# Kernel optimization log

Hardware: AMD Instinct MI355X
Metric: run time of the kernel (lower is better)

The kernel has to match this reference:

```python
import jax, jax.numpy as jnp
import numpy as np

N = 8192
D_IN = 512
D_HID = 256
D_OUT = 128
NEG_SLOPE = 0.25
MASK_VAL = -1.0e12
EDGE_PROB = 0.004  # avg degree ~33


def _leaky(x):
    return jax.nn.leaky_relu(x, NEG_SLOPE)


def setup_inputs() -> dict:
    key = jax.random.key(0)
    ks = jax.random.split(key, 9)
    x = jax.random.normal(ks[0], (N, D_IN), jnp.float32)
    # sparse-ish normalized adjacency, stored dense (torch uses sparse mm / to_dense)
    vals = jax.random.uniform(ks[1], (N, N), jnp.float32)
    mask = jax.random.uniform(ks[2], (N, N)) < EDGE_PROB
    adj = jnp.where(mask, vals, 0.0).astype(jnp.float32)
    W1 = jax.random.normal(ks[3], (D_IN, D_HID), jnp.float32) * (2.0 / (D_IN + D_HID)) ** 0.5
    b1 = jnp.zeros((D_HID,), jnp.float32)
    W2 = jax.random.normal(ks[4], (D_HID, D_HID), jnp.float32) * (1.0 / D_HID) ** 0.5
    b2 = jnp.zeros((D_HID,), jnp.float32)
    Wg = jax.random.normal(ks[5], (D_HID, D_OUT), jnp.float32) * (2.0 / (D_HID + D_OUT)) ** 0.5
    a = jax.random.normal(ks[6], (2 * D_OUT, 1), jnp.float32) * 0.1
    return dict(x=x, adj=adj, W1=W1, b1=b1, W2=W2, b2=b2, Wg=Wg, a=a)


def reference(x, adj, W1, b1, W2, b2, Wg, a):
    # GCN layer 1: adj @ (x @ W1) + b1, leaky_relu (dropout p=0 / eval -> identity)
    x1 = _leaky(adj @ (x @ W1) + b1)
    # GCN layer 2
    x2 = _leaky(adj @ (x1 @ W2) + b2)
    # GAT layer: h = x2 @ Wg; e[i,j] = leaky_relu([h_i || h_j] @ a)
    # identical to leaky_relu((h@a1)_i + (h@a2)_j) without the O(N^2*2F) concat
    h = x2 @ Wg                              # [N, D_OUT]
    a1 = a[:D_OUT, 0]
    a2 = a[D_OUT:, 0]
    e = _leaky((h @ a1)[:, None] + (h @ a2)[None, :])  # [N, N]
    att = jnp.where(adj > 0, e, MASK_VAL)
    att = jax.nn.softmax(att, axis=1)
    h_prime = att @ h                        # [N, D_OUT] (concat=False -> no elu)
    out = _leaky(h_prime)
    mu = out[:, : D_OUT // 2]
    logvar = out[:, D_OUT // 2 :]
    return mu, logvar
```

## Files before the change

kernel.cpp:

```cpp
#include <hip/hip_runtime.h>

typedef unsigned short u16;
typedef u16 u16x4 __attribute__((ext_vector_type(4)));
typedef __bf16 bf16x8 __attribute__((ext_vector_type(8)));
typedef float f32x4 __attribute__((ext_vector_type(4)));

#define NROW 8192
#define CAP 128
#define D_IN 512
#define D_HID 256
#define D_OUT 128

__device__ __forceinline__ float leaky_f(float x) { return x > 0.f ? x : 0.25f * x; }

__device__ __forceinline__ u16 f2bf_rne(float f) {
  unsigned u = __float_as_uint(f);
  u += 0x7fffu + ((u >> 16) & 1u);
  return (u16)(u >> 16);
}
__device__ __forceinline__ float bf2f(u16 v) { return __uint_as_float(((unsigned)v) << 16); }
__device__ __forceinline__ void split_bf16(float f, u16& hi, u16& lo) {
  hi = f2bf_rne(f);
  float fh = __uint_as_float(((unsigned)hi) << 16);
  lo = f2bf_rne(f - fh);
}

__global__ __launch_bounds__(256) void k_packw(
    const float* __restrict__ W1, u16* __restrict__ B1,
    const float* __restrict__ W2, u16* __restrict__ B2,
    const float* __restrict__ Wg, u16* __restrict__ B3) {
  const float* W; u16* Bt; int K, Nc, idx;
  int pb = blockIdx.x;
  if (pb < 64)      { W = W1; Bt = B1; K = D_IN;  Nc = D_HID; idx = pb * 256 + threadIdx.x; }
  else if (pb < 96) { W = W2; Bt = B2; K = D_HID; Nc = D_HID; idx = (pb - 64) * 256 + threadIdx.x; }
  else              { W = Wg; Bt = B3; K = D_HID; Nc = D_OUT; idx = (pb - 96) * 256 + threadIdx.x; }
  int ko8 = K >> 3;
  int n = idx / ko8, k0 = (idx % ko8) << 3;
  alignas(16) u16 hh[8], ll[8];
#pragma unroll
  for (int j = 0; j < 8; ++j) {
    float f = W[(size_t)(k0 + j) * Nc + n];
    split_bf16(f, hh[j], ll[j]);
  }
  size_t ro = (size_t)n * 2 * K;
  *(uint4*)(Bt + ro + k0)     = *(const uint4*)hh;
  *(uint4*)(Bt + ro + K + k0) = *(const uint4*)ll;
}

__global__ __launch_bounds__(256) void k_csr_gemm1(const float* __restrict__ adj,
    int* __restrict__ cnt, int* __restrict__ cols, float* __restrict__ vals,
    const float* __restrict__ X, const u16* __restrict__ Bt, float* __restrict__ C) {
  __shared__ u16 Ah[64 * 40], Al[64 * 40];
  __shared__ u16 Bh[64 * 40], Bl[64 * 40];
  __shared__ int csrc;
  int b = blockIdx.x;
  int tid = threadIdx.x;
  if (b < 512) {
    const int N = D_HID, K = D_IN;
    int bm = (b >> 2) * 64, bn = (b & 3) * 64;
    int wave = tid >> 6, lane = tid & 63, l15 = lane & 15, quad = lane >> 4;
    f32x4 acc[4] = {};
    int ar = tid >> 2, aj = (tid & 3) << 3;
    const float* Xrow = X + (size_t)(bm + ar) * K + aj;
    const u16* Brow = Bt + (size_t)(bn + ar) * (2 * K) + aj;
    for (int k0 = 0; k0 < K; k0 += 32) {
      alignas(16) u16 hh[8], ll[8];
      float xv[8];
      *(float4*)(xv)     = *(const float4*)(Xrow + k0);
      *(float4*)(xv + 4) = *(const float4*)(Xrow + k0 + 4);
#pragma unroll
      for (int e = 0; e < 8; ++e) split_bf16(xv[e], hh[e], ll[e]);
      *(uint4*)(&Ah[ar * 40 + aj]) = *(const uint4*)hh;
      *(uint4*)(&Al[ar * 40 + aj]) = *(const uint4*)ll;
      *(uint4*)(&Bh[ar * 40 + aj]) = *(const uint4*)(Brow + k0);
      *(uint4*)(&Bl[ar * 40 + aj]) = *(const uint4*)(Brow + K + k0);
      __syncthreads();
      bf16x8 afh = *(const bf16x8*)(&Ah[(wave * 16 + l15) * 40 + quad * 8]);
      bf16x8 afl = *(const bf16x8*)(&Al[(wave * 16 + l15) * 40 + quad * 8]);
#pragma unroll
      for (int c = 0; c < 4; ++c) {
        bf16x8 bfh = *(const bf16x8*)(&Bh[(c * 16 + l15) * 40 + quad * 8]);
        bf16x8 bfl = *(const bf16x8*)(&Bl[(c * 16 + l15) * 40 + quad * 8]);
        acc[c] = __builtin_amdgcn_mfma_f32_16x16x32_bf16(afh, bfh, acc[c], 0, 0, 0);
        acc[c] = __builtin_amdgcn_mfma_f32_16x16x32_bf16(afh, bfl, acc[c], 0, 0, 0);
        acc[c] = __builtin_amdgcn_mfma_f32_16x16x32_bf16(afl, bfh, acc[c], 0, 0, 0);
      }
      __syncthreads();
    }
#pragma unroll
    for (int c = 0; c < 4; ++c)
#pragma unroll
      for (int rg = 0; rg < 4; ++rg) {
        int rowi = bm + wave * 16 + quad * 4 + rg;
        int coli = bn + c * 16 + l15;
        C[(size_t)rowi * N + coli] = acc[c][rg];
      }
    return;
  }
  int i = b - 512;
  if (tid == 0) csrc = 0;
  __syncthreads();
  const float4* row = (const float4*)(adj + (size_t)i * NROW);
  for (int j4 = tid; j4 < NROW / 4; j4 += 256) {
    float4 v = row[j4];
    int base = j4 * 4;
    if (v.x > 0.f) { int s = atomicAdd(&csrc, 1); if (s < CAP) { cols[i*CAP+s] = base;   vals[i*CAP+s] = v.x; } }
    if (v.y > 0.f) { int s = atomicAdd(&csrc, 1); if (s < CAP) { cols[i*CAP+s] = base+1; vals[i*CAP+s] = v.y; } }
    if (v.z > 0.f) { int s = atomicAdd(&csrc, 1); if (s < CAP) { cols[i*CAP+s] = base+2; vals[i*CAP+s] = v.z; } }
    if (v.w > 0.f) { int s = atomicAdd(&csrc, 1); if (s < CAP) { cols[i*CAP+s] = base+3; vals[i*CAP+s] = v.w; } }
  }
  __syncthreads();
  if (tid == 0) cnt[i] = (csrc < CAP) ? csrc : CAP;
}

__global__ __launch_bounds__(256) void k_gemm(const u16* __restrict__ A, const u16* __restrict__ Bt,
    float* __restrict__ C, int N, int K) {
  __shared__ u16 Ah[64 * 40], Al[64 * 40];
  __shared__ u16 Bh[64 * 40], Bl[64 * 40];
  int tid = threadIdx.x;
  int bm = blockIdx.y * 64, bn = blockIdx.x * 64;
  int wave = tid >> 6, lane = tid & 63, l15 = lane & 15, quad = lane >> 4;
  f32x4 acc[4] = {};
  int ar = tid >> 2, aj = (tid & 3) << 3;
  const u16* Arow = A + (size_t)(bm + ar) * (2 * K) + aj;
  const u16* Brow = Bt + (size_t)(bn + ar) * (2 * K) + aj;
  for (int k0 = 0; k0 < K; k0 += 32) {
    *(uint4*)(&Ah[ar * 40 + aj]) = *(const uint4*)(Arow + k0);
    *(uint4*)(&Al[ar * 40 + aj]) = *(const uint4*)(Arow + K + k0);
    *(uint4*)(&Bh[ar * 40 + aj]) = *(const uint4*)(Brow + k0);
    *(uint4*)(&Bl[ar * 40 + aj]) = *(const uint4*)(Brow + K + k0);
    __syncthreads();
    bf16x8 afh = *(const bf16x8*)(&Ah[(wave * 16 + l15) * 40 + quad * 8]);
    bf16x8 afl = *(const bf16x8*)(&Al[(wave * 16 + l15) * 40 + quad * 8]);
#pragma unroll
    for (int c = 0; c < 4; ++c) {
      bf16x8 bfh = *(const bf16x8*)(&Bh[(c * 16 + l15) * 40 + quad * 8]);
      bf16x8 bfl = *(const bf16x8*)(&Bl[(c * 16 + l15) * 40 + quad * 8]);
      acc[c] = __builtin_amdgcn_mfma_f32_16x16x32_bf16(afh, bfh, acc[c], 0, 0, 0);
      acc[c] = __builtin_amdgcn_mfma_f32_16x16x32_bf16(afh, bfl, acc[c], 0, 0, 0);
      acc[c] = __builtin_amdgcn_mfma_f32_16x16x32_bf16(afl, bfh, acc[c], 0, 0, 0);
    }
    __syncthreads();
  }
#pragma unroll
  for (int c = 0; c < 4; ++c)
#pragma unroll
    for (int rg = 0; rg < 4; ++rg) {
      int rowi = bm + wave * 16 + quad * 4 + rg;
      int coli = bn + c * 16 + l15;
      C[(size_t)rowi * N + coli] = acc[c][rg];
    }
}

__global__ __launch_bounds__(256) void k_gemm3(const u16* __restrict__ A, const u16* __restrict__ Bt,
    u16* __restrict__ Hb, int K,
    const float* __restrict__ aptr, float* __restrict__ s1, float* __restrict__ s2) {
  __shared__ u16 Ah[32 * 40], Al[32 * 40];
  __shared__ u16 Bh[128 * 40], Bl[128 * 40];
  __shared__ float sp1[2][32], sp2[2][32];
  int tid = threadIdx.x;
  int bm = blockIdx.y * 32;
  int wave = tid >> 6, lane = tid & 63, l15 = lane & 15, quad = lane >> 4;
  int rhalf = wave >> 1, chalf = wave & 1;
  f32x4 acc[4] = {};
  int t7 = tid & 127;
  int ar = t7 >> 2, aj = (t7 & 3) << 3;
  int br = tid >> 1, bj = (tid & 1) << 4;
  const u16* Arow = A + (size_t)(bm + ar) * (2 * K) + aj + (tid < 128 ? 0 : K);
  u16* Adst = (tid < 128 ? Ah : Al) + ar * 40 + aj;
  const u16* Brow = Bt + (size_t)br * (2 * K) + bj;
  for (int k0 = 0; k0 < K; k0 += 32) {
    *(uint4*)Adst = *(const uint4*)(Arow + k0);
#pragma unroll
    for (int jj = 0; jj < 2; ++jj) {
      *(uint4*)(&Bh[br * 40 + bj + jj * 8]) = *(const uint4*)(Brow + k0 + jj * 8);
      *(uint4*)(&Bl[br * 40 + bj + jj * 8]) = *(const uint4*)(Brow + K + k0 + jj * 8);
    }
    __syncthreads();
    bf16x8 afh = *(const bf16x8*)(&Ah[(rhalf * 16 + l15) * 40 + quad * 8]);
    bf16x8 afl = *(const bf16x8*)(&Al[(rhalf * 16 + l15) * 40 + quad * 8]);
#pragma unroll
    for (int c = 0; c < 4; ++c) {
      bf16x8 bfh = *(const bf16x8*)(&Bh[(chalf * 64 + c * 16 + l15) * 40 + quad * 8]);
      bf16x8 bfl = *(const bf16x8*)(&Bl[(chalf * 64 + c * 16 + l15) * 40 + quad * 8]);
      acc[c] = __builtin_amdgcn_mfma_f32_16x16x32_bf16(afh, bfh, acc[c], 0, 0, 0);
      acc[c] = __builtin_amdgcn_mfma_f32_16x16x32_bf16(afh, bfl, acc[c], 0, 0, 0);
      acc[c] = __builtin_amdgcn_mfma_f32_16x16x32_bf16(afl, bfh, acc[c], 0, 0, 0);
    }
    __syncthreads();
  }
#pragma unroll
  for (int c = 0; c < 4; ++c)
#pragma unroll
    for (int rg = 0; rg < 4; ++rg) {
      int rowi = bm + rhalf * 16 + quad * 4 + rg;
      int coli = chalf * 64 + c * 16 + l15;
      Hb[(size_t)rowi * 128 + coli] = f2bf_rne(acc[c][rg]);
    }
  float a1v[4], a2v[4];
#pragma unroll
  for (int c = 0; c < 4; ++c) {
    a1v[c] = aptr[chalf * 64 + c * 16 + l15];
    a2v[c] = aptr[128 + chalf * 64 + c * 16 + l15];
  }
#pragma unroll
  for (int rg = 0; rg < 4; ++rg) {
    float p1 = 0.f, p2 = 0.f;
#pragma unroll
    for (int c = 0; c < 4; ++c) { p1 = fmaf(acc[c][rg], a1v[c], p1); p2 = fmaf(acc[c][rg], a2v[c], p2); }
#pragma unroll
    for (int m = 1; m < 16; m <<= 1) { p1 += __shfl_xor(p1, m); p2 += __shfl_xor(p2, m); }
    if (l15 == 0) {
      int rloc = rhalf * 16 + quad * 4 + rg;
      sp1[chalf][rloc] = p1; sp2[chalf][rloc] = p2;
    }
  }
  __syncthreads();
  if (tid < 32) {
    s1[bm + tid] = sp1[0][tid] + sp1[1][tid];
    s2[bm + tid] = sp2[0][tid] + sp2[1][tid];
  }
}

__global__ __launch_bounds__(256) void k_spmm_pack(const float* __restrict__ Hin,
    const float* __restrict__ bias, const int* __restrict__ cnt,
    const int* __restrict__ cols, const float* __restrict__ vals, u16* __restrict__ Ap) {
  int i = blockIdx.x, t = threadIdx.x;
  int t64 = t & 63, g = t >> 6;
  __shared__ int sc[CAP];
  __shared__ float sv[CAP];
  __shared__ float4 sacc[4][64];
  int n = cnt[i];
  if (t < n) { sc[t] = cols[i * CAP + t]; sv[t] = vals[i * CAP + t]; }
  __syncthreads();
  float4 acc = {0.f, 0.f, 0.f, 0.f};
  const float4* H4 = (const float4*)Hin;
  for (int k = g; k < n; k += 4) {
    float w = sv[k];
    float4 v = H4[(size_t)sc[k] * 64 + t64];
    acc.x = fmaf(w, v.x, acc.x); acc.y = fmaf(w, v.y, acc.y);
    acc.z = fmaf(w, v.z, acc.z); acc.w = fmaf(w, v.w, acc.w);
  }
  sacc[g][t64] = acc;
  __syncthreads();
  if (t < 64) {
    float4 a0 = sacc[0][t], a1 = sacc[1][t], a2 = sacc[2][t], a3 = sacc[3][t];
    float4 bv = ((const float4*)bias)[t];
    float r[4] = { leaky_f(a0.x + a1.x + a2.x + a3.x + bv.x),
                   leaky_f(a0.y + a1.y + a2.y + a3.y + bv.y),
                   leaky_f(a0.z + a1.z + a2.z + a3.z + bv.z),
                   leaky_f(a0.w + a1.w + a2.w + a3.w + bv.w) };
    u16x4 hi4, lo4;
#pragma unroll
    for (int e = 0; e < 4; ++e) { u16 hh, ll; split_bf16(r[e], hh, ll); hi4[e] = hh; lo4[e] = ll; }
    size_t ro = (size_t)i * 512;
    *(u16x4*)(Ap + ro + 4 * t) = hi4;
    *(u16x4*)(Ap + ro + 256 + 4 * t) = lo4;
  }
}

__global__ __launch_bounds__(128) void k_attn(const u16* __restrict__ Hb,
    const float* __restrict__ s1, const float* __restrict__ s2,
    const int* __restrict__ cnt, const int* __restrict__ cols, float* __restrict__ out) {
  int i = blockIdx.x, t = threadIdx.x;
  int t32 = t & 31, g = t >> 5;
  __shared__ int sc[CAP];
  __shared__ float sw[CAP];
  __shared__ float sred[2];
  __shared__ float4 sacc[4][32];
  int n = cnt[i];
  float s1i = s1[i];
  if (t < n) { int c = cols[i * CAP + t]; sc[t] = c; sw[t] = leaky_f(s1i + s2[c]); }
  __syncthreads();
  if (t < 64) {
    float m = -1e30f;
    if (t < n) m = sw[t];
    if (t + 64 < n) m = fmaxf(m, sw[t + 64]);
    for (int o = 32; o > 0; o >>= 1) m = fmaxf(m, __shfl_down(m, o));
    if (t == 0) sred[0] = m;
  }
  __syncthreads();
  float mx = sred[0];
  if (t < n) sw[t] = expf(sw[t] - mx);
  __syncthreads();
  if (t < 64) {
    float s = 0.f;
    if (t < n) s = sw[t];
    if (t + 64 < n) s += sw[t + 64];
    for (int o = 32; o > 0; o >>= 1) s += __shfl_down(s, o);
    if (t == 0) sred[1] = s;
  }
  __syncthreads();
  float inv = (n > 0) ? 1.0f / sred[1] : 0.f;
  float4 acc = {0.f, 0.f, 0.f, 0.f};
  for (int k = g; k < n; k += 4) {
    float w = sw[k];
    u16x4 v = *(const u16x4*)(Hb + (size_t)sc[k] * 128 + 4 * t32);
    acc.x = fmaf(w, bf2f(v[0]), acc.x); acc.y = fmaf(w, bf2f(v[1]), acc.y);
    acc.z = fmaf(w, bf2f(v[2]), acc.z); acc.w = fmaf(w, bf2f(v[3]), acc.w);
  }
  sacc[g][t32] = acc;
  __syncthreads();
  if (t < 32) {
    float4 a0 = sacc[0][t], a1 = sacc[1][t], a2 = sacc[2][t], a3 = sacc[3][t];
    float4 r;
    r.x = leaky_f((a0.x + a1.x + a2.x + a3.x) * inv);
    r.y = leaky_f((a0.y + a1.y + a2.y + a3.y) * inv);
    r.z = leaky_f((a0.z + a1.z + a2.z + a3.z) * inv);
    r.w = leaky_f((a0.w + a1.w + a2.w + a3.w) * inv);
    float4* o4 = (float4*)out;
    if (t < 16) o4[(size_t)i * 16 + t] = r;
    else        o4[(size_t)NROW * 16 + (size_t)i * 16 + (t - 16)] = r;
  }
}

extern "C" void kernel_launch(void* const* d_in, const int* in_sizes, int n_in,
                              void* d_out, int out_size, void* d_ws, size_t ws_size,
                              hipStream_t stream) {
  const float* x   = (const float*)d_in[0];
  const float* adj = (const float*)d_in[1];
  const float* W1  = (const float*)d_in[2];
  const float* b1  = (const float*)d_in[3];
  const float* W2  = (const float*)d_in[4];
  const float* b2  = (const float*)d_in[5];
  const float* Wg  = (const float*)d_in[6];
  const float* a   = (const float*)d_in[7];
  float* out = (float*)d_out;

  char* ws = (char*)d_ws;
  int*   row_cnt  = (int*)  (ws + 0);
  int*   row_cols = (int*)  (ws + 32768);
  float* row_vals = (float*)(ws + 4227072);
  u16*   B1t      = (u16*)  (ws + 8421376);
  u16*   B2t      = (u16*)  (ws + 8945664);
  u16*   B3t      = (u16*)  (ws + 9207808);
  float* s1       = (float*)(ws + 9338880);
  float* s2       = (float*)(ws + 9371648);
  u16*   hbf      = (u16*)  (ws + 9404416);
  float* H0T2     = (float*)(ws + 13598720);
  u16*   Apack    = (u16*)  (ws + 21987328);

  k_packw<<<112, 256, 0, stream>>>(W1, B1t, W2, B2t, Wg, B3t);
  k_csr_gemm1<<<512 + NROW, 256, 0, stream>>>(adj, row_cnt, row_cols, row_vals, x, B1t, H0T2);
  k_spmm_pack<<<NROW, 256, 0, stream>>>(H0T2, b1, row_cnt, row_cols, row_vals, Apack);
  k_gemm<<<dim3(4, 128), 256, 0, stream>>>(Apack, B2t, H0T2, D_HID, D_HID);
  k_spmm_pack<<<NROW, 256, 0, stream>>>(H0T2, b2, row_cnt, row_cols, row_vals, Apack);
  k_gemm3<<<dim3(1, 256), 256, 0, stream>>>(Apack, B3t, hbf, D_HID, a, s1, s2);
  k_attn<<<NROW, 128, 0, stream>>>(hbf, s1, s2, row_cnt, row_cols, out);
}
```

Before: 472.9 us.

## Map one row per wavefront in SpMM and attention kernels with unrolled gathers

The sparse aggregation and attention kernels now assign one row to each 64-lane wavefront, with four rows per block, instead of a whole block per row. This removes the shared-memory cross-group reductions and most block barriers, and the softmax max and sum reductions now run within a wave using shuffles. The gather loops are unrolled by 8 (or 4 per half-wave) to keep more independent loads in flight. In exchange, each wave handles its row serially over all neighbours, so per-row latency grows with degree.

```diff
diff --git a/kernel.cpp b/kernel.cpp
--- a/kernel.cpp
+++ b/kernel.cpp
@@ -225,92 +225,118 @@
 __global__ __launch_bounds__(256) void k_spmm_pack(const float* __restrict__ Hin,
     const float* __restrict__ bias, const int* __restrict__ cnt,
     const int* __restrict__ cols, const float* __restrict__ vals, u16* __restrict__ Ap) {
-  int i = blockIdx.x, t = threadIdx.x;
-  int t64 = t & 63, g = t >> 6;
-  __shared__ int sc[CAP];
-  __shared__ float sv[CAP];
-  __shared__ float4 sacc[4][64];
+  __shared__ int sc[4][CAP];
+  __shared__ float sv[4][CAP];
+  int w = threadIdx.x >> 6, lane = threadIdx.x & 63;
+  int i = blockIdx.x * 4 + w;
   int n = cnt[i];
-  if (t < n) { sc[t] = cols[i * CAP + t]; sv[t] = vals[i * CAP + t]; }
-  __syncthreads();
+  if (lane < n)      { sc[w][lane]      = cols[i * CAP + lane];      sv[w][lane]      = vals[i * CAP + lane]; }
+  if (lane + 64 < n) { sc[w][lane + 64] = cols[i * CAP + lane + 64]; sv[w][lane + 64] = vals[i * CAP + lane + 64]; }
+  __syncthreads();
+  const float4* H4 = (const float4*)Hin;
   float4 acc = {0.f, 0.f, 0.f, 0.f};
-  const float4* H4 = (const float4*)Hin;
-  for (int k = g; k < n; k += 4) {
-    float w = sv[k];
-    float4 v = H4[(size_t)sc[k] * 64 + t64];
-    acc.x = fmaf(w, v.x, acc.x); acc.y = fmaf(w, v.y, acc.y);
-    acc.z = fmaf(w, v.z, acc.z); acc.w = fmaf(w, v.w, acc.w);
-  }
-  sacc[g][t64] = acc;
-  __syncthreads();
-  if (t < 64) {
-    float4 a0 = sacc[0][t], a1 = sacc[1][t], a2 = sacc[2][t], a3 = sacc[3][t];
-    float4 bv = ((const float4*)bias)[t];
-    float r[4] = { leaky_f(a0.x + a1.x + a2.x + a3.x + bv.x),
-                   leaky_f(a0.y + a1.y + a2.y + a3.y + bv.y),
-                   leaky_f(a0.z + a1.z + a2.z + a3.z + bv.z),
-                   leaky_f(a0.w + a1.w + a2.w + a3.w + bv.w) };
-    u16x4 hi4, lo4;
-#pragma unroll
-    for (int e = 0; e < 4; ++e) { u16 hh, ll; split_bf16(r[e], hh, ll); hi4[e] = hh; lo4[e] = ll; }
-    size_t ro = (size_t)i * 512;
-    *(u16x4*)(Ap + ro + 4 * t) = hi4;
-    *(u16x4*)(Ap + ro + 256 + 4 * t) = lo4;
-  }
-}
-
-__global__ __launch_bounds__(128) void k_attn(const u16* __restrict__ Hb,
+  int k = 0;
+  for (; k + 7 < n; k += 8) {
+    int   c0 = sc[w][k],     c1 = sc[w][k + 1], c2 = sc[w][k + 2], c3 = sc[w][k + 3];
+    int   c4 = sc[w][k + 4], c5 = sc[w][k + 5], c6 = sc[w][k + 6], c7 = sc[w][k + 7];
+    float w0 = sv[w][k],     w1 = sv[w][k + 1], w2 = sv[w][k + 2], w3 = sv[w][k + 3];
+    float w4 = sv[w][k + 4], w5 = sv[w][k + 5], w6 = sv[w][k + 6], w7 = sv[w][k + 7];
+    float4 v0 = H4[(size_t)c0 * 64 + lane];
+    float4 v1 = H4[(size_t)c1 * 64 + lane];
+    float4 v2 = H4[(size_t)c2 * 64 + lane];
+    float4 v3 = H4[(size_t)c3 * 64 + lane];
+    float4 v4 = H4[(size_t)c4 * 64 + lane];
+    float4 v5 = H4[(size_t)c5 * 64 + lane];
+    float4 v6 = H4[(size_t)c6 * 64 + lane];
+    float4 v7 = H4[(size_t)c7 * 64 + lane];
+    acc.x = fmaf(w0, v0.x, acc.x); acc.y = fmaf(w0, v0.y, acc.y); acc.z = fmaf(w0, v0.z, acc.z); acc.w = fmaf(w0, v0.w, acc.w);
+    acc.x = fmaf(w1, v1.x, acc.x); acc.y = fmaf(w1, v1.y, acc.y); acc.z = fmaf(w1, v1.z, acc.z); acc.w = fmaf(w1, v1.w, acc.w);
+    acc.x = fmaf(w2, v2.x, acc.x); acc.y = fmaf(w2, v2.y, acc.y); acc.z = fmaf(w2, v2.z, acc.z); acc.w = fmaf(w2, v2.w, acc.w);
+    acc.x = fmaf(w3, v3.x, acc.x); acc.y = fmaf(w3, v3.y, acc.y); acc.z = fmaf(w3, v3.z, acc.z); acc.w = fmaf(w3, v3.w, acc.w);
+    acc.x = fmaf(w4, v4.x, acc.x); acc.y = fmaf(w4, v4.y, acc.y); acc.z = fmaf(w4, v4.z, acc.z); acc.w = fmaf(w4, v4.w, acc.w);
+    acc.x = fmaf(w5, v5.x, acc.x); acc.y = fmaf(w5, v5.y, acc.y); acc.z = fmaf(w5, v5.z, acc.z); acc.w = fmaf(w5, v5.w, acc.w);
+    acc.x = fmaf(w6, v6.x, acc.x); acc.y = fmaf(w6, v6.y, acc.y); acc.z = fmaf(w6, v6.z, acc.z); acc.w = fmaf(w6, v6.w, acc.w);
+    acc.x = fmaf(w7, v7.x, acc.x); acc.y = fmaf(w7, v7.y, acc.y); acc.z = fmaf(w7, v7.z, acc.z); acc.w = fmaf(w7, v7.w, acc.w);
+  }
+  for (; k < n; ++k) {
+    float wv = sv[w][k];
+    float4 v = H4[(size_t)sc[w][k] * 64 + lane];
+    acc.x = fmaf(wv, v.x, acc.x); acc.y = fmaf(wv, v.y, acc.y);
+    acc.z = fmaf(wv, v.z, acc.z); acc.w = fmaf(wv, v.w, acc.w);
+  }
+  float4 bv = ((const float4*)bias)[lane];
+  float r[4] = { leaky_f(acc.x + bv.x), leaky_f(acc.y + bv.y),
+                 leaky_f(acc.z + bv.z), leaky_f(acc.w + bv.w) };
+  u16x4 hi4, lo4;
+#pragma unroll
+  for (int e = 0; e < 4; ++e) { u16 hh, ll; split_bf16(r[e], hh, ll); hi4[e] = hh; lo4[e] = ll; }
+  size_t ro = (size_t)i * 512;
+  *(u16x4*)(Ap + ro + 4 * lane) = hi4;
+  *(u16x4*)(Ap + ro + 256 + 4 * lane) = lo4;
+}
+
+__global__ __launch_bounds__(256) void k_attn(const u16* __restrict__ Hb,
     const float* __restrict__ s1, const float* __restrict__ s2,
     const int* __restrict__ cnt, const int* __restrict__ cols, float* __restrict__ out) {
-  int i = blockIdx.x, t = threadIdx.x;
-  int t32 = t & 31, g = t >> 5;
-  __shared__ int sc[CAP];
-  __shared__ float sw[CAP];
-  __shared__ float sred[2];
-  __shared__ float4 sacc[4][32];
+  __shared__ int sc[4][CAP];
+  __shared__ float sp[4][CAP];
+  int w = threadIdx.x >> 6, lane = threadIdx.x & 63;
+  int i = blockIdx.x * 4 + w;
   int n = cnt[i];
   float s1i = s1[i];
-  if (t < n) { int c = cols[i * CAP + t]; sc[t] = c; sw[t] = leaky_f(s1i + s2[c]); }
-  __syncthreads();
-  if (t < 64) {
-    float m = -1e30f;
-    if (t < n) m = sw[t];
-    if (t + 64 < n) m = fmaxf(m, sw[t + 64]);
-    for (int o = 32; o > 0; o >>= 1) m = fmaxf(m, __shfl_down(m, o));
-    if (t == 0) sred[0] = m;
-  }
-  __syncthreads();
-  float mx = sred[0];
-  if (t < n) sw[t] = expf(sw[t] - mx);
-  __syncthreads();
-  if (t < 64) {
-    float s = 0.f;
-    if (t < n) s = sw[t];
-    if (t + 64 < n) s += sw[t + 64];
-    for (int o = 32; o > 0; o >>= 1) s += __shfl_down(s, o);
-    if (t == 0) sred[1] = s;
-  }
-  __syncthreads();
-  float inv = (n > 0) ? 1.0f / sred[1] : 0.f;
+  float e0 = -1e30f, e1 = -1e30f;
+  if (lane < n)      { int c = cols[i * CAP + lane];      sc[w][lane]      = c; e0 = leaky_f(s1i + s2[c]); }
+  if (lane + 64 < n) { int c = cols[i * CAP + lane + 64]; sc[w][lane + 64] = c; e1 = leaky_f(s1i + s2[c]); }
+  float m = fmaxf(e0, e1);
+#pragma unroll
+  for (int o = 32; o > 0; o >>= 1) m = fmaxf(m, __shfl_xor(m, o));
+  float p0 = (lane < n)      ? expf(e0 - m) : 0.f;
+  float p1 = (lane + 64 < n) ? expf(e1 - m) : 0.f;
+  if (lane < n)      sp[w][lane]      = p0;
+  if (lane + 64 < n) sp[w][lane + 64] = p1;
+  float s = p0 + p1;
+#pragma unroll
+  for (int o = 32; o > 0; o >>= 1) s += __shfl_xor(s, o);
+  float inv = (n > 0) ? 1.0f / s : 0.f;
+  __syncthreads();
+  int half = lane >> 5, t32 = lane & 31;
   float4 acc = {0.f, 0.f, 0.f, 0.f};
-  for (int k = g; k < n; k += 4) {
-    float w = sw[k];
-    u16x4 v = *(const u16x4*)(Hb + (size_t)sc[k] * 128 + 4 * t32);
-    acc.x = fmaf(w, bf2f(v[0]), acc.x); acc.y = fmaf(w, bf2f(v[1]), acc.y);
-    acc.z = fmaf(w, bf2f(v[2]), acc.z); acc.w = fmaf(w, bf2f(v[3]), acc.w);
-  }
-  sacc[g][t32] = acc;
-  __syncthreads();
-  if (t < 32) {
-    float4 a0 = sacc[0][t], a1 = sacc[1][t], a2 = sacc[2][t], a3 = sacc[3][t];
+  int k = half;
+  for (; k + 6 < n; k += 8) {
+    int   c0 = sc[w][k],     c1 = sc[w][k + 2], c2 = sc[w][k + 4], c3 = sc[w][k + 6];
+    float w0 = sp[w][k],     w1 = sp[w][k + 2], w2 = sp[w][k + 4], w3 = sp[w][k + 6];
+    u16x4 a0 = *(const u16x4*)(Hb + (size_t)c0 * 128 + 4 * t32);
+    u16x4 a1 = *(const u16x4*)(Hb + (size_t)c1 * 128 + 4 * t32);
+    u16x4 a2 = *(const u16x4*)(Hb + (size_t)c2 * 128 + 4 * t32);
+    u16x4 a3 = *(const u16x4*)(Hb + (size_t)c3 * 128 + 4 * t32);
+    acc.x = fmaf(w0, bf2f(a0[0]), acc.x); acc.y = fmaf(w0, bf2f(a0[1]), acc.y);
+    acc.z = fmaf(w0, bf2f(a0[2]), acc.z); acc.w = fmaf(w0, bf2f(a0[3]), acc.w);
+    acc.x = fmaf(w1, bf2f(a1[0]), acc.x); acc.y = fmaf(w1, bf2f(a1[1]), acc.y);
+    acc.z = fmaf(w1, bf2f(a1[2]), acc.z); acc.w = fmaf(w1, bf2f(a1[3]), acc.w);
+    acc.x = fmaf(w2, bf2f(a2[0]), acc.x); acc.y = fmaf(w2, bf2f(a2[1]), acc.y);
+    acc.z = fmaf(w2, bf2f(a2[2]), acc.z); acc.w = fmaf(w2, bf2f(a2[3]), acc.w);
+    acc.x = fmaf(w3, bf2f(a3[0]), acc.x); acc.y = fmaf(w3, bf2f(a3[1]), acc.y);
+    acc.z = fmaf(w3, bf2f(a3[2]), acc.z); acc.w = fmaf(w3, bf2f(a3[3]), acc.w);
+  }
+  for (; k < n; k += 2) {
+    float wv = sp[w][k];
+    u16x4 a = *(const u16x4*)(Hb + (size_t)sc[w][k] * 128 + 4 * t32);
+    acc.x = fmaf(wv, bf2f(a[0]), acc.x); acc.y = fmaf(wv, bf2f(a[1]), acc.y);
+    acc.z = fmaf(wv, bf2f(a[2]), acc.z); acc.w = fmaf(wv, bf2f(a[3]), acc.w);
+  }
+  acc.x += __shfl_xor(acc.x, 32);
+  acc.y += __shfl_xor(acc.y, 32);
+  acc.z += __shfl_xor(acc.z, 32);
+  acc.w += __shfl_xor(acc.w, 32);
+  if (lane < 32) {
     float4 r;
-    r.x = leaky_f((a0.x + a1.x + a2.x + a3.x) * inv);
-    r.y = leaky_f((a0.y + a1.y + a2.y + a3.y) * inv);
-    r.z = leaky_f((a0.z + a1.z + a2.z + a3.z) * inv);
-    r.w = leaky_f((a0.w + a1.w + a2.w + a3.w) * inv);
+    r.x = leaky_f(acc.x * inv);
+    r.y = leaky_f(acc.y * inv);
+    r.z = leaky_f(acc.z * inv);
+    r.w = leaky_f(acc.w * inv);
     float4* o4 = (float4*)out;
-    if (t < 16) o4[(size_t)i * 16 + t] = r;
-    else        o4[(size_t)NROW * 16 + (size_t)i * 16 + (t - 16)] = r;
+    if (lane < 16) o4[(size_t)i * 16 + lane] = r;
+    else           o4[(size_t)NROW * 16 + (size_t)i * 16 + (lane - 16)] = r;
   }
 }
 
@@ -342,9 +368,9 @@
 
   k_packw<<<112, 256, 0, stream>>>(W1, B1t, W2, B2t, Wg, B3t);
   k_csr_gemm1<<<512 + NROW, 256, 0, stream>>>(adj, row_cnt, row_cols, row_vals, x, B1t, H0T2);
-  k_spmm_pack<<<NROW, 256, 0, stream>>>(H0T2, b1, row_cnt, row_cols, row_vals, Apack);
+  k_spmm_pack<<<NROW / 4, 256, 0, stream>>>(H0T2, b1, row_cnt, row_cols, row_vals, Apack);
   k_gemm<<<dim3(4, 128), 256, 0, stream>>>(Apack, B2t, H0T2, D_HID, D_HID);
-  k_spmm_pack<<<NROW, 256, 0, stream>>>(H0T2, b2, row_cnt, row_cols, row_vals, Apack);
+  k_spmm_pack<<<NROW / 4, 256, 0, stream>>>(H0T2, b2, row_cnt, row_cols, row_vals, Apack);
   k_gemm3<<<dim3(1, 256), 256, 0, stream>>>(Apack, B3t, hbf, D_HID, a, s1, s2);
-  k_attn<<<NROW, 128, 0, stream>>>(hbf, s1, s2, row_cnt, row_cols, out);
-}
+  k_attn<<<NROW / 4, 256, 0, stream>>>(hbf, s1, s2, row_cnt, row_cols, out);
+}
```

Result: faster. 463.5 us (-2.0%).
